# Optimization experiments

Hardware: AMD Instinct MI355X
Metric: run time of the kernel (lower is better)

The kernel has to match this reference:

```python
import jax, jax.numpy as jnp
import numpy as np

N_LAYERS = 4

def setup_inputs() -> dict:
    key = jax.random.key(0)
    ks = jax.random.split(key, 5)
    B, T, V, E, H = 32, 64, 32000, 1024, 1024
    return {
        "batch_target_in": jax.random.randint(ks[0], (B, T), 0, V, dtype=jnp.int32),
        "states": jnp.zeros((2 * N_LAYERS, B, H), jnp.float32),  # h0,c0,h1,c1,...
        "emb": jax.random.normal(ks[1], (V, E), jnp.float32) * 0.05,
        "Wx": jax.random.normal(ks[2], (N_LAYERS, H, 4 * H), jnp.float32) * 0.05,
        "Wh": jax.random.normal(ks[3], (N_LAYERS, H, 4 * H), jnp.float32) * 0.05,
        "b": jnp.zeros((N_LAYERS, 4 * H), jnp.float32),
        "Wfc": jax.random.normal(ks[4], (H, V), jnp.float32) * 0.05,
        "bfc": jnp.zeros((V,), jnp.float32),
    }

def reference(batch_target_in, states, emb, Wx, Wh, b, Wfc, bfc):
    # Embedding lookup: [B, T, E] -> time-major [T, B, E]
    x = jnp.swapaxes(emb[batch_target_in], 0, 1)
    h0 = states[0::2]  # [L, B, H]
    c0 = states[1::2]  # [L, B, H]

    def step(carry, x_t):
        h, c = carry
        inp = x_t
        hs, cs = [], []
        for l in range(N_LAYERS):
            # Keras LSTM gate order: i, f, c(g), o
            z = inp @ Wx[l] + h[l] @ Wh[l] + b[l]        # [B, 4H]
            i, f, g, o = jnp.split(z, 4, axis=-1)
            c_new = jax.nn.sigmoid(f) * c[l] + jax.nn.sigmoid(i) * jnp.tanh(g)
            h_new = jax.nn.sigmoid(o) * jnp.tanh(c_new)
            hs.append(h_new)
            cs.append(c_new)
            inp = h_new  # dropout rate 0 -> identity
        return (jnp.stack(hs), jnp.stack(cs)), hs[-1]

    _, tops = jax.lax.scan(step, (h0, c0), x)            # tops: [T, B, H]
    logits = jnp.einsum('tbh,hv->tbv', tops, Wfc) + bfc  # [T, B, V]
    probs = jax.nn.softmax(logits, axis=-1)
    return jnp.swapaxes(probs, 0, 1)                     # [B, T, V]
```

## Files before the change

kernel.cpp:

```cpp
#include <hip/hip_runtime.h>
#include <stdint.h>


#define NL 4
#define BB 32
#define TT 64
#define HH 1024
#define VV 32000

typedef __attribute__((ext_vector_type(8))) short bf16x8;
typedef __attribute__((ext_vector_type(4))) float f32x4;

__device__ __forceinline__ unsigned short f2bf(float f) {
  union { float f; unsigned u; } v; v.f = f;
  unsigned u = v.u;
  u = u + 0x7fffu + ((u >> 16) & 1u);
  return (unsigned short)(u >> 16);
}

__global__ void __launch_bounds__(256)
swizzle_w(const float* __restrict__ src, unsigned short* __restrict__ dst,
          int K, int N, int mode, long long src_lstride, long long dst_lstride) {
  int l = blockIdx.z;
  src += (long long)l * src_lstride;
  dst += (long long)l * dst_lstride;
  int k0  = blockIdx.x * 64;
  int ntb = blockIdx.y;
  __shared__ float lds[64][65];
  int tid = threadIdx.x;
  for (int it = 0; it < 16; ++it) {
    int idx = tid + it * 256;
    int kk = idx >> 6;
    int cl = idx & 63;
    int col;
    if (mode == 1) col = ((cl >> 4) << 10) + ntb * 16 + (cl & 15);
    else           col = ntb * 64 + cl;
    lds[kk][cl] = src[(long long)(k0 + kk) * N + col];
  }
  __syncthreads();
  int kqn = K >> 5;
  for (int p = 0; p < 2; ++p) {
    int o = tid + p * 256;
    int lane = o & 63;
    int kql  = (o >> 6) & 1;
    int ntl  = o >> 7;
    int i = lane & 15;
    int kloc = kql * 32 + ((lane >> 4) << 3);
    int clocal;
    if (mode == 1) clocal = ((i >> 2) << 4) + ntl * 4 + (i & 3);
    else           clocal = ntl * 16 + i;
    unsigned short o8[8] __attribute__((aligned(16)));
    #pragma unroll
    for (int j = 0; j < 8; ++j) o8[j] = f2bf(lds[kloc + j][clocal]);
    int nt = ntb * 4 + ntl;
    int kq = (k0 >> 5) + kql;
    long long doff = ((((long long)nt * kqn) + kq) << 9) + (lane << 3);
    *reinterpret_cast<uint4*>(dst + doff) = *reinterpret_cast<const uint4*>(o8);
  }
}

__global__ void __launch_bounds__(256)
embed_swz(const int* __restrict__ tok, const float* __restrict__ emb,
          unsigned short* __restrict__ xsw) {
  int gid = blockIdx.x * 256 + threadIdx.x;
  int lane = gid & 63;
  int kq = (gid >> 6) & 31;
  int rt = (gid >> 11) & 1;
  int t  = gid >> 12;
  int r = rt * 16 + (lane & 15);
  int k = kq * 32 + (((lane >> 4) & 3) << 3);
  int token = tok[r * TT + t];
  const float* s = emb + (long long)token * HH + k;
  unsigned short o8[8] __attribute__((aligned(16)));
  #pragma unroll
  for (int j = 0; j < 8; ++j) o8[j] = f2bf(s[j]);
  long long off = (long long)t * 32768 + (((rt * 32 + kq) * 64 + lane) << 3);
  *reinterpret_cast<uint4*>(xsw + off) = *reinterpret_cast<const uint4*>(o8);
}

__global__ void __launch_bounds__(256)
init_h(const float* __restrict__ states, unsigned short* __restrict__ hsw) {
  int gid = blockIdx.x * 256 + threadIdx.x;
  int lane = gid & 63;
  int kq = (gid >> 6) & 31;
  int rt = (gid >> 11) & 1;
  int l  = gid >> 12;
  int r = rt * 16 + (lane & 15);
  int k = kq * 32 + (((lane >> 4) & 3) << 3);
  const float* hs = states + (long long)(2 * l) * (BB * HH) + r * HH + k;
  unsigned short o8[8] __attribute__((aligned(16)));
  #pragma unroll
  for (int j = 0; j < 8; ++j) o8[j] = f2bf(hs[j]);
  long long off = (long long)(l * 2 + 1) * 32768 + (((rt * 32 + kq) * 64 + lane) << 3);
  *reinterpret_cast<uint4*>(hsw + off) = *reinterpret_cast<const uint4*>(o8);
}

__global__ void __launch_bounds__(512, 2)
lstm_kernel(const unsigned short* __restrict__ Wsw,
            const float* __restrict__ bias,
            const unsigned short* __restrict__ xsw,
            unsigned short* hsw,
            const float* __restrict__ states,
            unsigned short* topsw,
            unsigned* sync) {
  const int tid  = threadIdx.x;
  const int wave = tid >> 6;
  const int lane = tid & 63;
  const int bid  = blockIdx.x;
  const int layer = bid & 3;
  const int g     = bid >> 2;
  const int mat  = wave >> 2;
  const int kqb  = (wave & 3) << 3;

  __shared__ float zsh[8][64][34];

  bf16x8 wreg[4][8];
  #pragma unroll
  for (int ct = 0; ct < 4; ++ct) {
    const unsigned short* wb =
        Wsw + ((((long long)(layer * 2 + mat) * 256 + (g * 4 + ct)) * 32 + kqb) << 9)
            + (lane << 3);
    #pragma unroll
    for (int s = 0; s < 8; ++s)
      wreg[ct][s] = *reinterpret_cast<const bf16x8*>(wb + (s << 9));
  }

  const int r    = tid & 31;
  const int jj   = tid >> 5;
  const int jcol = g * 16 + jj;
  float cR = states[(long long)(2 * layer + 1) * (BB * HH) + r * HH + jcol];
  float bia[4];
  #pragma unroll
  for (int q = 0; q < 4; ++q) bia[q] = bias[(layer << 12) + (q << 10) + jcol];

  const int i4 = (lane >> 4) << 2;
  const int rl = lane & 15;
  const int hrt = r >> 4, hkq = jcol >> 5;
  const int hln = (r & 15) | (((jcol >> 3) & 3) << 4);
  const int hoff = (((hrt << 5) | hkq) << 9) | (hln << 3) | (jcol & 7);
  const int zb = ((jj >> 2) << 4) + (jj & 3);

  unsigned* grp = sync + 64 + ((bid >> 5) << 5);

  const int ND = TT + NL - 1;
  for (int d = 0; d < ND; ++d) {
    const int t = d - layer;
    if (t >= 0 && t < TT) {
      const unsigned short* ibase;
      if (mat == 0)
        ibase = (layer == 0) ? (xsw + (long long)t * 32768)
                             : (hsw + (long long)((layer - 1) * 2 + (t & 1)) * 32768);
      else
        ibase = hsw + (long long)(layer * 2 + ((t + 1) & 1)) * 32768;
      ibase += (kqb << 9) + (lane << 3);

      f32x4 acc[4][2];
      #pragma unroll
      for (int ct = 0; ct < 4; ++ct) {
        acc[ct][0] = (f32x4){0.f, 0.f, 0.f, 0.f};
        acc[ct][1] = (f32x4){0.f, 0.f, 0.f, 0.f};
      }
      #pragma unroll
      for (int s = 0; s < 8; ++s) {
        bf16x8 b0 = *reinterpret_cast<const bf16x8*>(ibase + (s << 9));
        bf16x8 b1 = *reinterpret_cast<const bf16x8*>(ibase + 16384 + (s << 9));
        #pragma unroll
        for (int ct = 0; ct < 4; ++ct) {
          acc[ct][0] = __builtin_amdgcn_mfma_f32_16x16x32_bf16(wreg[ct][s], b0, acc[ct][0], 0, 0, 0);
          acc[ct][1] = __builtin_amdgcn_mfma_f32_16x16x32_bf16(wreg[ct][s], b1, acc[ct][1], 0, 0, 0);
        }
      }
      #pragma unroll
      for (int ct = 0; ct < 4; ++ct) {
        #pragma unroll
        for (int reg = 0; reg < 4; ++reg) {
          zsh[wave][ct * 16 + i4 + reg][rl]      = acc[ct][0][reg];
          zsh[wave][ct * 16 + i4 + reg][16 + rl] = acc[ct][1][reg];
        }
      }
      __syncthreads();
      {
        float zg[4];
        #pragma unroll
        for (int q = 0; q < 4; ++q) {
          int zr = zb + (q << 2);
          float z = 0.f;
          #pragma unroll
          for (int w = 0; w < 8; ++w) z += zsh[w][zr][r];
          zg[q] = z + bia[q];
        }
        float si = 1.f / (1.f + __expf(-zg[0]));
        float sf = 1.f / (1.f + __expf(-zg[1]));
        float so = 1.f / (1.f + __expf(-zg[3]));
        float e2 = __expf(-2.f * fabsf(zg[2]));
        float tg = (1.f - e2) / (1.f + e2);
        tg = zg[2] < 0.f ? -tg : tg;
        float cnew = sf * cR + si * tg;
        cR = cnew;
        float e2c = __expf(-2.f * fabsf(cnew));
        float th = (1.f - e2c) / (1.f + e2c);
        th = cnew < 0.f ? -th : th;
        unsigned short hb = f2bf(so * th);
        hsw[(long long)(layer * 2 + (t & 1)) * 32768 + hoff] = hb;
        if (layer == 3) topsw[(long long)t * 32768 + hoff] = hb;
      }
    }
    if (d == ND - 1) break;
    __syncthreads();
    if (tid == 0) {
      unsigned step = (unsigned)(d + 1);
      unsigned old = __hip_atomic_fetch_add(grp, 1u, __ATOMIC_RELEASE,
                                            __HIP_MEMORY_SCOPE_AGENT);
      if (old == 32u * step - 1u) {
        (void)__hip_atomic_load(grp, __ATOMIC_ACQUIRE, __HIP_MEMORY_SCOPE_AGENT);
        unsigned o2 = __hip_atomic_fetch_add(sync + 32, 1u, __ATOMIC_RELEASE,
                                             __HIP_MEMORY_SCOPE_AGENT);
        if (o2 == 8u * step - 1u) {
          (void)__hip_atomic_load(sync + 32, __ATOMIC_ACQUIRE, __HIP_MEMORY_SCOPE_AGENT);
          __hip_atomic_store(sync, step, __ATOMIC_RELEASE, __HIP_MEMORY_SCOPE_AGENT);
        }
      }
      while (__hip_atomic_load(sync, __ATOMIC_RELAXED, __HIP_MEMORY_SCOPE_AGENT) < step)
        __builtin_amdgcn_s_sleep(2);
      (void)__hip_atomic_load(sync, __ATOMIC_ACQUIRE, __HIP_MEMORY_SCOPE_AGENT);
    }
    __syncthreads();
  }
}

__global__ void __launch_bounds__(256)
final_gemm(const unsigned short* __restrict__ topsw,
           const unsigned short* __restrict__ wfcsw,
           const float* __restrict__ bfc,
           float* __restrict__ out) {
  int tid = threadIdx.x, wave = tid >> 6, lane = tid & 63;
  int mtb = blockIdx.y * 8;
  int ntb = blockIdx.x * 16 + wave * 4;
  f32x4 acc[8][4];
  #pragma unroll
  for (int i = 0; i < 8; ++i)
    #pragma unroll
    for (int n = 0; n < 4; ++n) acc[i][n] = (f32x4){0.f, 0.f, 0.f, 0.f};
  const unsigned short* abase = topsw + (((long long)mtb * 32) << 9) + (lane << 3);
  const unsigned short* bbase = wfcsw + (((long long)ntb * 32) << 9) + (lane << 3);
  for (int kq = 0; kq < 32; ++kq) {
    bf16x8 bf[4];
    #pragma unroll
    for (int n = 0; n < 4; ++n)
      bf[n] = *reinterpret_cast<const bf16x8*>(bbase + (((n * 32 + kq)) << 9));
    #pragma unroll
    for (int i = 0; i < 8; ++i) {
      bf16x8 af = *reinterpret_cast<const bf16x8*>(abase + (((i * 32 + kq)) << 9));
      #pragma unroll
      for (int n = 0; n < 4; ++n)
        acc[i][n] = __builtin_amdgcn_mfma_f32_16x16x32_bf16(af, bf[n], acc[i][n], 0, 0, 0);
    }
  }
  int i4 = (lane >> 4) << 2;
  int nl = lane & 15;
  #pragma unroll
  for (int i = 0; i < 8; ++i) {
    int mt = mtb + i;
    #pragma unroll
    for (int n = 0; n < 4; ++n) {
      int v = (ntb + n) * 16 + nl;
      float bv = bfc[v];
      #pragma unroll
      for (int reg = 0; reg < 4; ++reg) {
        int m = mt * 16 + i4 + reg;
        int b = m & 31, t = m >> 5;
        out[((long long)b * TT + t) * VV + v] = acc[i][n][reg] + bv;
      }
    }
  }
}

__global__ void __launch_bounds__(256)
softmax_k(float* __restrict__ out) {
  float* p = out + (long long)blockIdx.x * VV;
  int tid = threadIdx.x;
  __shared__ float red[24];
  float m = -1e30f;
  for (int i = tid; i < VV; i += 256) m = fmaxf(m, p[i]);
  #pragma unroll
  for (int o = 32; o > 0; o >>= 1) m = fmaxf(m, __shfl_down(m, o, 64));
  if ((tid & 63) == 0) red[tid >> 6] = m;
  __syncthreads();
  if (tid == 0) red[8] = fmaxf(fmaxf(red[0], red[1]), fmaxf(red[2], red[3]));
  __syncthreads();
  float mm = red[8];
  float s = 0.f;
  for (int i = tid; i < VV; i += 256) s += __expf(p[i] - mm);
  #pragma unroll
  for (int o = 32; o > 0; o >>= 1) s += __shfl_down(s, o, 64);
  if ((tid & 63) == 0) red[16 + (tid >> 6)] = s;
  __syncthreads();
  if (tid == 0) red[9] = 1.f / (red[16] + red[17] + red[18] + red[19]);
  __syncthreads();
  float inv = red[9];
  for (int i = tid; i < VV; i += 256) p[i] = __expf(p[i] - mm) * inv;
}

extern "C" void kernel_launch(void* const* d_in, const int* in_sizes, int n_in,
                              void* d_out, int out_size, void* d_ws, size_t ws_size,
                              hipStream_t stream) {
  const int*   tok    = (const int*)  d_in[0];
  const float* states = (const float*)d_in[1];
  const float* emb    = (const float*)d_in[2];
  const float* Wx     = (const float*)d_in[3];
  const float* Wh     = (const float*)d_in[4];
  const float* bias   = (const float*)d_in[5];
  const float* Wfc    = (const float*)d_in[6];
  const float* bfc    = (const float*)d_in[7];
  float* out = (float*)d_out;

  char* ws = (char*)d_ws;
  unsigned* sync = (unsigned*)ws;
  size_t off = 2048;
  unsigned short* Wsw   = (unsigned short*)(ws + off); off += (size_t)8 * 1024 * 4096 * 2;
  unsigned short* Wfcsw = (unsigned short*)(ws + off); off += (size_t)VV * HH * 2;
  unsigned short* xsw   = (unsigned short*)(ws + off); off += (size_t)TT * 32768 * 2;
  unsigned short* topsw = (unsigned short*)(ws + off); off += (size_t)TT * 32768 * 2;
  unsigned short* hsw   = (unsigned short*)(ws + off); off += (size_t)8 * 32768 * 2;

  hipMemsetAsync(sync, 0, 2048, stream);

  swizzle_w<<<dim3(16, 64, 4), 256, 0, stream>>>(
      Wx, Wsw, HH, 4 * HH, 1, (long long)HH * 4 * HH, (long long)2 * HH * 4 * HH);
  swizzle_w<<<dim3(16, 64, 4), 256, 0, stream>>>(
      Wh, Wsw + (size_t)HH * 4 * HH, HH, 4 * HH, 1,
      (long long)HH * 4 * HH, (long long)2 * HH * 4 * HH);
  swizzle_w<<<dim3(16, 500, 1), 256, 0, stream>>>(Wfc, Wfcsw, HH, VV, 0, 0, 0);

  embed_swz<<<1024, 256, 0, stream>>>(tok, emb, xsw);
  init_h<<<64, 256, 0, stream>>>(states, hsw);

  lstm_kernel<<<256, 512, 0, stream>>>(Wsw, bias, xsw, hsw, states, topsw, sync);

  final_gemm<<<dim3(125, 16), 256, 0, stream>>>(topsw, Wfcsw, bfc, out);
  softmax_k<<<BB * TT, 256, 0, stream>>>(out);
}
```

Before: 2.040 ms.

## Replace global wavefront barrier with per-layer dataflow counters and single-pass softmax

The LSTM kernel no longer uses a grid-wide barrier on every diagonal step. Each layer's 64 blocks now wait only on per-(layer, timestep) counters for their own previous step and the layer below. To avoid overwrite hazards when layers run at different paces, the hidden-state buffer is expanded to hold all T+1 timesteps per layer. Softmax is rewritten as an online max/sum pass with float4 loads, so it reads the row twice instead of three times. The cost is a larger workspace, more counters to zero, and relaxed atomic stores of h that rely on the release fetch_add for visibility.

```diff
diff --git a/kernel.cpp b/kernel.cpp
--- a/kernel.cpp
+++ b/kernel.cpp
@@ -91,7 +91,7 @@
   unsigned short o8[8] __attribute__((aligned(16)));
   #pragma unroll
   for (int j = 0; j < 8; ++j) o8[j] = f2bf(hs[j]);
-  long long off = (long long)(l * 2 + 1) * 32768 + (((rt * 32 + kq) * 64 + lane) << 3);
+  long long off = (long long)(l * (TT + 1)) * 32768 + (((rt * 32 + kq) * 64 + lane) << 3);
   *reinterpret_cast<uint4*>(hsw + off) = *reinterpret_cast<const uint4*>(o8);
 }
 
@@ -140,91 +140,90 @@
   const int hoff = (((hrt << 5) | hkq) << 9) | (hln << 3) | (jcol & 7);
   const int zb = ((jj >> 2) << 4) + (jj & 3);
 
-  unsigned* grp = sync + 64 + ((bid >> 5) << 5);
-
-  const int ND = TT + NL - 1;
-  for (int d = 0; d < ND; ++d) {
-    const int t = d - layer;
-    if (t >= 0 && t < TT) {
-      const unsigned short* ibase;
-      if (mat == 0)
-        ibase = (layer == 0) ? (xsw + (long long)t * 32768)
-                             : (hsw + (long long)((layer - 1) * 2 + (t & 1)) * 32768);
-      else
-        ibase = hsw + (long long)(layer * 2 + ((t + 1) & 1)) * 32768;
-      ibase += (kqb << 9) + (lane << 3);
-
-      f32x4 acc[4][2];
+  for (int t = 0; t < TT; ++t) {
+    if (t > 0 && tid == 0) {
+      const unsigned* c0 = sync + ((layer * TT + (t - 1)) << 4);
+      while (__hip_atomic_load(c0, __ATOMIC_RELAXED, __HIP_MEMORY_SCOPE_AGENT) < 64u)
+        __builtin_amdgcn_s_sleep(1);
+    }
+    if (layer > 0 && tid == 64) {
+      const unsigned* c1 = sync + (((layer - 1) * TT + t) << 4);
+      while (__hip_atomic_load(c1, __ATOMIC_RELAXED, __HIP_MEMORY_SCOPE_AGENT) < 64u)
+        __builtin_amdgcn_s_sleep(1);
+    }
+    __syncthreads();
+
+    const unsigned short* ibase;
+    if (mat == 0)
+      ibase = (layer == 0) ? (xsw + (long long)t * 32768)
+                           : (hsw + (long long)((layer - 1) * (TT + 1) + t + 1) * 32768);
+    else
+      ibase = hsw + (long long)(layer * (TT + 1) + t) * 32768;
+    ibase += (kqb << 9) + (lane << 3);
+
+    f32x4 acc[4][2];
+    #pragma unroll
+    for (int ct = 0; ct < 4; ++ct) {
+      acc[ct][0] = (f32x4){0.f, 0.f, 0.f, 0.f};
+      acc[ct][1] = (f32x4){0.f, 0.f, 0.f, 0.f};
+    }
+    #pragma unroll
+    for (int s = 0; s < 8; ++s) {
+      bf16x8 b0 = *reinterpret_cast<const bf16x8*>(ibase + (s << 9));
+      bf16x8 b1 = *reinterpret_cast<const bf16x8*>(ibase + 16384 + (s << 9));
       #pragma unroll
       for (int ct = 0; ct < 4; ++ct) {
-        acc[ct][0] = (f32x4){0.f, 0.f, 0.f, 0.f};
-        acc[ct][1] = (f32x4){0.f, 0.f, 0.f, 0.f};
+        acc[ct][0] = __builtin_amdgcn_mfma_f32_16x16x32_bf16(wreg[ct][s], b0, acc[ct][0], 0, 0, 0);
+        acc[ct][1] = __builtin_amdgcn_mfma_f32_16x16x32_bf16(wreg[ct][s], b1, acc[ct][1], 0, 0, 0);
       }
-      #pragma unroll
-      for (int s = 0; s < 8; ++s) {
-        bf16x8 b0 = *reinterpret_cast<const bf16x8*>(ibase + (s << 9));
-        bf16x8 b1 = *reinterpret_cast<const bf16x8*>(ibase + 16384 + (s << 9));
-        #pragma unroll
-        for (int ct = 0; ct < 4; ++ct) {
-          acc[ct][0] = __builtin_amdgcn_mfma_f32_16x16x32_bf16(wreg[ct][s], b0, acc[ct][0], 0, 0, 0);
-          acc[ct][1] = __builtin_amdgcn_mfma_f32_16x16x32_bf16(wreg[ct][s], b1, acc[ct][1], 0, 0, 0);
-        }
+    }
+    #pragma unroll
+    for (int ct = 0; ct < 4; ++ct) {
+      #pragma unroll
+      for (int reg = 0; reg < 4; ++reg) {
+        zsh[wave][ct * 16 + i4 + reg][rl]      = acc[ct][0][reg];
+        zsh[wave][ct * 16 + i4 + reg][16 + rl] = acc[ct][1][reg];
       }
-      #pragma unroll
-      for (int ct = 0; ct < 4; ++ct) {
-        #pragma unroll
-        for (int reg = 0; reg < 4; ++reg) {
-          zsh[wave][ct * 16 + i4 + reg][rl]      = acc[ct][0][reg];
-          zsh[wave][ct * 16 + i4 + reg][16 + rl] = acc[ct][1][reg];
-        }
-      }
-      __syncthreads();
-      {
-        float zg[4];
-        #pragma unroll
-        for (int q = 0; q < 4; ++q) {
-          int zr = zb + (q << 2);
-          float z = 0.f;
-          #pragma unroll
-          for (int w = 0; w < 8; ++w) z += zsh[w][zr][r];
-          zg[q] = z + bia[q];
-        }
-        float si = 1.f / (1.f + __expf(-zg[0]));
-        float sf = 1.f / (1.f + __expf(-zg[1]));
-        float so = 1.f / (1.f + __expf(-zg[3]));
-        float e2 = __expf(-2.f * fabsf(zg[2]));
-        float tg = (1.f - e2) / (1.f + e2);
-        tg = zg[2] < 0.f ? -tg : tg;
-        float cnew = sf * cR + si * tg;
-        cR = cnew;
-        float e2c = __expf(-2.f * fabsf(cnew));
-        float th = (1.f - e2c) / (1.f + e2c);
-        th = cnew < 0.f ? -th : th;
-        unsigned short hb = f2bf(so * th);
-        hsw[(long long)(layer * 2 + (t & 1)) * 32768 + hoff] = hb;
-        if (layer == 3) topsw[(long long)t * 32768 + hoff] = hb;
-      }
-    }
-    if (d == ND - 1) break;
+    }
     __syncthreads();
-    if (tid == 0) {
-      unsigned step = (unsigned)(d + 1);
-      unsigned old = __hip_atomic_fetch_add(grp, 1u, __ATOMIC_RELEASE,
-                                            __HIP_MEMORY_SCOPE_AGENT);
-      if (old == 32u * step - 1u) {
-        (void)__hip_atomic_load(grp, __ATOMIC_ACQUIRE, __HIP_MEMORY_SCOPE_AGENT);
-        unsigned o2 = __hip_atomic_fetch_add(sync + 32, 1u, __ATOMIC_RELEASE,
-                                             __HIP_MEMORY_SCOPE_AGENT);
-        if (o2 == 8u * step - 1u) {
-          (void)__hip_atomic_load(sync + 32, __ATOMIC_ACQUIRE, __HIP_MEMORY_SCOPE_AGENT);
-          __hip_atomic_store(sync, step, __ATOMIC_RELEASE, __HIP_MEMORY_SCOPE_AGENT);
-        }
-      }
-      while (__hip_atomic_load(sync, __ATOMIC_RELAXED, __HIP_MEMORY_SCOPE_AGENT) < step)
-        __builtin_amdgcn_s_sleep(2);
-      (void)__hip_atomic_load(sync, __ATOMIC_ACQUIRE, __HIP_MEMORY_SCOPE_AGENT);
-    }
+
+    float zg[4];
+    #pragma unroll
+    for (int q = 0; q < 4; ++q) {
+      int zr = zb + (q << 2);
+      float z = 0.f;
+      #pragma unroll
+      for (int w = 0; w < 8; ++w) z += zsh[w][zr][r];
+      zg[q] = z + bia[q];
+    }
+    float si = 1.f / (1.f + __expf(-zg[0]));
+    float sf = 1.f / (1.f + __expf(-zg[1]));
+    float so = 1.f / (1.f + __expf(-zg[3]));
+    float e2 = __expf(-2.f * fabsf(zg[2]));
+    float tg = (1.f - e2) / (1.f + e2);
+    tg = zg[2] < 0.f ? -tg : tg;
+    float cnew = sf * cR + si * tg;
+    cR = cnew;
+    float e2c = __expf(-2.f * fabsf(cnew));
+    float th = (1.f - e2c) / (1.f + e2c);
+    th = cnew < 0.f ? -th : th;
+    unsigned short hb = f2bf(so * th);
+
+    unsigned hv = (unsigned)hb;
+    unsigned pv = (unsigned)__shfl_xor((int)hv, 32, 64);
+    if ((tid & 32) == 0) {
+      unsigned u = hv | (pv << 16);
+      unsigned* hdst = (unsigned*)(hsw + (long long)(layer * (TT + 1) + t + 1) * 32768);
+      __hip_atomic_store(hdst + (hoff >> 1), u, __ATOMIC_RELAXED,
+                         __HIP_MEMORY_SCOPE_AGENT);
+      if (layer == 3)
+        ((unsigned*)(topsw + (long long)t * 32768))[hoff >> 1] = u;
+    }
+
     __syncthreads();
+    if (tid == 0)
+      __hip_atomic_fetch_add(sync + ((layer * TT + t) << 4), 1u,
+                             __ATOMIC_RELEASE, __HIP_MEMORY_SCOPE_AGENT);
   }
 }
 
@@ -277,28 +276,46 @@
 
 __global__ void __launch_bounds__(256)
 softmax_k(float* __restrict__ out) {
-  float* p = out + (long long)blockIdx.x * VV;
+  float4* p4 = reinterpret_cast<float4*>(out + (long long)blockIdx.x * VV);
   int tid = threadIdx.x;
-  __shared__ float red[24];
-  float m = -1e30f;
-  for (int i = tid; i < VV; i += 256) m = fmaxf(m, p[i]);
-  #pragma unroll
-  for (int o = 32; o > 0; o >>= 1) m = fmaxf(m, __shfl_down(m, o, 64));
-  if ((tid & 63) == 0) red[tid >> 6] = m;
+  __shared__ float redm[4], reds[4], fin[2];
+  float m = -1e30f, s = 0.f;
+  for (int i = tid; i < VV / 4; i += 256) {
+    float4 v = p4[i];
+    float lm = fmaxf(fmaxf(v.x, v.y), fmaxf(v.z, v.w));
+    if (lm > m) { s *= __expf(m - lm); m = lm; }
+    s += __expf(v.x - m) + __expf(v.y - m) + __expf(v.z - m) + __expf(v.w - m);
+  }
+  #pragma unroll
+  for (int o = 32; o > 0; o >>= 1) {
+    float om = __shfl_down(m, o, 64);
+    float os = __shfl_down(s, o, 64);
+    float nm = fmaxf(m, om);
+    s = s * __expf(m - nm) + os * __expf(om - nm);
+    m = nm;
+  }
+  if ((tid & 63) == 0) { redm[tid >> 6] = m; reds[tid >> 6] = s; }
   __syncthreads();
-  if (tid == 0) red[8] = fmaxf(fmaxf(red[0], red[1]), fmaxf(red[2], red[3]));
+  if (tid == 0) {
+    float M = redm[0], S = reds[0];
+    #pragma unroll
+    for (int w = 1; w < 4; ++w) {
+      float nm = fmaxf(M, redm[w]);
+      S = S * __expf(M - nm) + reds[w] * __expf(redm[w] - nm);
+      M = nm;
+    }
+    fin[0] = M; fin[1] = 1.f / S;
+  }
   __syncthreads();
-  float mm = red[8];
-  float s = 0.f;
-  for (int i = tid; i < VV; i += 256) s += __expf(p[i] - mm);
-  #pragma unroll
-  for (int o = 32; o > 0; o >>= 1) s += __shfl_down(s, o, 64);
-  if ((tid & 63) == 0) red[16 + (tid >> 6)] = s;
-  __syncthreads();
-  if (tid == 0) red[9] = 1.f / (red[16] + red[17] + red[18] + red[19]);
-  __syncthreads();
-  float inv = red[9];
-  for (int i = tid; i < VV; i += 256) p[i] = __expf(p[i] - mm) * inv;
+  float M = fin[0], inv = fin[1];
+  for (int i = tid; i < VV / 4; i += 256) {
+    float4 v = p4[i];
+    v.x = __expf(v.x - M) * inv;
+    v.y = __expf(v.y - M) * inv;
+    v.z = __expf(v.z - M) * inv;
+    v.w = __expf(v.w - M) * inv;
+    p4[i] = v;
+  }
 }
 
 extern "C" void kernel_launch(void* const* d_in, const int* in_sizes, int n_in,
@@ -316,14 +333,14 @@
 
   char* ws = (char*)d_ws;
   unsigned* sync = (unsigned*)ws;
-  size_t off = 2048;
+  size_t off = 32768;
   unsigned short* Wsw   = (unsigned short*)(ws + off); off += (size_t)8 * 1024 * 4096 * 2;
   unsigned short* Wfcsw = (unsigned short*)(ws + off); off += (size_t)VV * HH * 2;
   unsigned short* xsw   = (unsigned short*)(ws + off); off += (size_t)TT * 32768 * 2;
   unsigned short* topsw = (unsigned short*)(ws + off); off += (size_t)TT * 32768 * 2;
-  unsigned short* hsw   = (unsigned short*)(ws + off); off += (size_t)8 * 32768 * 2;
-
-  hipMemsetAsync(sync, 0, 2048, stream);
+  unsigned short* hsw   = (unsigned short*)(ws + off); off += (size_t)NL * (TT + 1) * 32768 * 2;
+
+  hipMemsetAsync(sync, 0, 32768, stream);
 
   swizzle_w<<<dim3(16, 64, 4), 256, 0, stream>>>(
       Wx, Wsw, HH, 4 * HH, 1, (long long)HH * 4 * HH, (long long)2 * HH * 4 * HH);
```

After: 1.693 ms. 17.0% less time.
